# Kernel tuning notes

Measured on AMD Instinct MI355X. Metric: run time of the kernel, lower is better.

## Reference

```python
import jax, jax.numpy as jnp
import numpy as np

TAU = 0.07
EPS = 1e-12  # matches torch F.normalize clamp_min eps


def setup_inputs() -> dict:
    key = jax.random.key(0)
    k1, k2 = jax.random.split(key)
    feat = jax.random.normal(k1, (4, 64, 512, 512), dtype=jnp.float32)
    gt = jax.random.randint(k2, (4, 19, 512, 512), 0, 2, dtype=jnp.int32)
    return {"feat": feat, "gt": gt}


def reference(feat, gt):
    # feat: [b, c, h, w], gt: [b, k, h, w] multi-hot in {0,1}
    mask = (gt == 1).astype(feat.dtype)                      # [b,k,h,w]
    num_pos = mask.sum()

    # Scatter-sum class prototypes: k0[k] = sum of feat at positive pixels of class k
    k0 = jnp.einsum('bkhw,bchw->kc', mask, feat)             # [k,c]
    k0n = k0 / jnp.maximum(jnp.linalg.norm(k0, axis=1, keepdims=True), EPS)

    # Per-pixel L2-normalized features over channel dim
    fn = feat / jnp.maximum(jnp.linalg.norm(feat, axis=1, keepdims=True), EPS)

    # Cosine similarity to every prototype, temperature-scaled softmax NLL over classes
    logits = jnp.einsum('kc,bchw->bkhw', k0n, fn) / TAU      # [b,k,h,w]
    logp = jax.nn.log_softmax(logits, axis=1)

    # Sum NLL over all (pixel, class) positive pairs; a pixel positive for
    # multiple classes contributes once per class, exactly like the loop.
    loss = -(mask * logp).sum() / num_pos
    return loss
```

## Files before the change

### kernel.cpp

```cpp
#include <hip/hip_runtime.h>
#include <cstdint>
#include <cstddef>

#define HW    262144
#define C     64
#define K     19
#define NPIX  1048576
#define TAUINV (1.0f / 0.07f)
#define EPS   1e-12f

#define NCHUNK (NPIX / 32)
#define CPB    8192
#define G1     1024


typedef __attribute__((ext_vector_type(8))) short bf16x8;
typedef __attribute__((ext_vector_type(4))) float f32x4;

__device__ __forceinline__ float wave_reduce_f32(float v) {
#pragma unroll
    for (int off = 32; off; off >>= 1) v += __shfl_down(v, off);
    return v;
}
__device__ __forceinline__ unsigned wave_reduce_u32(unsigned v) {
#pragma unroll
    for (int off = 32; off; off >>= 1) v += __shfl_down(v, off);
    return v;
}

__device__ __forceinline__ void split1(float f, short& h, short& l) {
    const unsigned u  = __float_as_uint(f);
    const unsigned hb = (u + 0x7FFFu + ((u >> 16) & 1u)) & 0xFFFF0000u;
    h = (short)(hb >> 16);
    const float lo = f - __uint_as_float(hb);
    const unsigned v = __float_as_uint(lo);
    l = (short)((v + 0x7FFFu + ((v >> 16) & 1u)) >> 16);
}

__global__ __launch_bounds__(256) void k1_proto(
    const float* __restrict__ feat, const int* __restrict__ gt,
    unsigned* __restrict__ pm,
    float* __restrict__ k0p, unsigned* __restrict__ num_pos)
{
    __shared__ float red[32 * 64];
    const int tid  = threadIdx.x;
    const int lane = tid & 63;
    const int wv   = tid >> 6;
    const int q    = lane >> 4;
    const int n    = lane & 15;
    const int q8   = q << 3;

    f32x4 acc[2][4];
#pragma unroll
    for (int mt = 0; mt < 2; ++mt)
#pragma unroll
        for (int nt = 0; nt < 4; ++nt)
            acc[mt][nt] = (f32x4){0.f, 0.f, 0.f, 0.f};
    unsigned npos = 0;

    const int wave_id = blockIdx.x * 4 + wv;
    const int nwaves  = G1 * 4;

    for (int chunk = wave_id; chunk < NCHUNK; chunk += nwaves) {
        const int b   = chunk >> 13;
        const int hw0 = (chunk & (CPB - 1)) << 5;
        const size_t fbase = (size_t)b * C * HW + hw0;

        unsigned mymask = 0;
        if (lane < 32) {
            const int* gp = gt + (size_t)b * K * HW + hw0 + lane;
#pragma unroll
            for (int k = 0; k < K; ++k)
                mymask |= (gp[(size_t)k * HW] == 1) ? (1u << k) : 0u;
            pm[(size_t)chunk * 32 + lane] = mymask;
            npos += __popc(mymask);
        }

        unsigned w8[8];
#pragma unroll
        for (int j = 0; j < 8; ++j) w8[j] = __shfl(mymask, q8 + j);
        bf16x8 a0, a1;
#pragma unroll
        for (int j = 0; j < 8; ++j) {
            a0[j] = (short)(((w8[j] >> n) & 1u) * 0x3F80u);
            a1[j] = (short)(((w8[j] >> (n + 16)) & 1u) * 0x3F80u);
        }

        const float* fp = feat + fbase + (size_t)n * HW + q8;
#pragma unroll
        for (int nt = 0; nt < 4; ++nt) {
            const float* p = fp + (size_t)(nt * 16) * HW;
            const float4 x = *(const float4*)p;
            const float4 y = *(const float4*)(p + 4);
            bf16x8 bh, bl;
            {
                short h, l;
                split1(x.x, h, l); bh[0] = h; bl[0] = l;
                split1(x.y, h, l); bh[1] = h; bl[1] = l;
                split1(x.z, h, l); bh[2] = h; bl[2] = l;
                split1(x.w, h, l); bh[3] = h; bl[3] = l;
                split1(y.x, h, l); bh[4] = h; bl[4] = l;
                split1(y.y, h, l); bh[5] = h; bl[5] = l;
                split1(y.z, h, l); bh[6] = h; bl[6] = l;
                split1(y.w, h, l); bh[7] = h; bl[7] = l;
            }
            acc[0][nt] = __builtin_amdgcn_mfma_f32_16x16x32_bf16(a0, bh, acc[0][nt], 0, 0, 0);
            acc[0][nt] = __builtin_amdgcn_mfma_f32_16x16x32_bf16(a0, bl, acc[0][nt], 0, 0, 0);
            acc[1][nt] = __builtin_amdgcn_mfma_f32_16x16x32_bf16(a1, bh, acc[1][nt], 0, 0, 0);
            acc[1][nt] = __builtin_amdgcn_mfma_f32_16x16x32_bf16(a1, bl, acc[1][nt], 0, 0, 0);
        }
    }

    for (int w = 0; w < 4; ++w) {
        if (wv == w) {
#pragma unroll
            for (int mt = 0; mt < 2; ++mt)
#pragma unroll
                for (int nt = 0; nt < 4; ++nt)
#pragma unroll
                    for (int r = 0; r < 4; ++r) {
                        const int idx = (mt * 16 + q * 4 + r) * 64 + nt * 16 + n;
                        if (w == 0) red[idx]  = acc[mt][nt][r];
                        else        red[idx] += acc[mt][nt][r];
                    }
        }
        __syncthreads();
    }
    for (int i = tid; i < 32 * 64; i += 256)
        atomicAdd(&k0p[i], red[i]);

    const unsigned np = wave_reduce_u32(npos);
    if (lane == 0) atomicAdd(num_pos, np);
}

__global__ __launch_bounds__(256) void k2_norm(
    const float* __restrict__ k0p, float* __restrict__ k0n)
{
    __shared__ float rn[K];
    const int tid  = threadIdx.x;
    const int lane = tid & 63;
    const int wv   = tid >> 6;
    for (int cls = wv; cls < K; cls += 4) {
        const float v = k0p[cls * 64 + lane];
        const float s = wave_reduce_f32(v * v);
        if (lane == 0) rn[cls] = 1.0f / fmaxf(sqrtf(s), EPS);
    }
    __syncthreads();
    for (int i = tid; i < K * 64; i += 256) k0n[i] = k0p[i] * rn[i >> 6];
}

__global__ __launch_bounds__(256) void k3_loss(
    const float* __restrict__ feat, const int* __restrict__ gt,
    const unsigned* __restrict__ pm, const float* __restrict__ k0n,
    float* __restrict__ loss_sum)
{
    __shared__ __align__(16) float w[K * 64];
    const int tid = threadIdx.x;
    for (int i = tid; i < K * 64; i += 256) w[i] = k0n[i];
    __syncthreads();

    const int px0 = (blockIdx.x * 256 + tid) << 2;
    const int b   = px0 >> 18;
    const int hw  = px0 & (HW - 1);
    const float* fb = feat + (size_t)b * C * HW + hw;

    unsigned marr[4];
    {
        const uint4 mv = *(const uint4*)(pm + px0);
        marr[0] = mv.x; marr[1] = mv.y; marr[2] = mv.z; marr[3] = mv.w;
    }

    float4 dot[K];
#pragma unroll
    for (int k = 0; k < K; ++k) dot[k] = make_float4(0.f, 0.f, 0.f, 0.f);
    float4 ss = make_float4(0.f, 0.f, 0.f, 0.f);

    float4 f[8];
#pragma unroll
    for (int j = 0; j < 8; ++j)
        f[j] = *(const float4*)(fb + (size_t)j * HW);

#pragma unroll
    for (int cg = 0; cg < 64; cg += 8) {
        float4 g[8];
        if (cg + 8 < 64) {
#pragma unroll
            for (int j = 0; j < 8; ++j)
                g[j] = *(const float4*)(fb + (size_t)(cg + 8 + j) * HW);
        }
#pragma unroll
        for (int j = 0; j < 8; ++j) {
            const float4 fv = f[j];
            ss.x = fmaf(fv.x, fv.x, ss.x); ss.y = fmaf(fv.y, fv.y, ss.y);
            ss.z = fmaf(fv.z, fv.z, ss.z); ss.w = fmaf(fv.w, fv.w, ss.w);
        }
#pragma unroll
        for (int k = 0; k < K; ++k) {
            const float4 wa = *(const float4*)&w[k * 64 + cg];
            const float4 wb = *(const float4*)&w[k * 64 + cg + 4];
            float4 d = dot[k];
            d.x = fmaf(f[0].x, wa.x, d.x); d.y = fmaf(f[0].y, wa.x, d.y);
            d.z = fmaf(f[0].z, wa.x, d.z); d.w = fmaf(f[0].w, wa.x, d.w);
            d.x = fmaf(f[1].x, wa.y, d.x); d.y = fmaf(f[1].y, wa.y, d.y);
            d.z = fmaf(f[1].z, wa.y, d.z); d.w = fmaf(f[1].w, wa.y, d.w);
            d.x = fmaf(f[2].x, wa.z, d.x); d.y = fmaf(f[2].y, wa.z, d.y);
            d.z = fmaf(f[2].z, wa.z, d.z); d.w = fmaf(f[2].w, wa.z, d.w);
            d.x = fmaf(f[3].x, wa.w, d.x); d.y = fmaf(f[3].y, wa.w, d.y);
            d.z = fmaf(f[3].z, wa.w, d.z); d.w = fmaf(f[3].w, wa.w, d.w);
            d.x = fmaf(f[4].x, wb.x, d.x); d.y = fmaf(f[4].y, wb.x, d.y);
            d.z = fmaf(f[4].z, wb.x, d.z); d.w = fmaf(f[4].w, wb.x, d.w);
            d.x = fmaf(f[5].x, wb.y, d.x); d.y = fmaf(f[5].y, wb.y, d.y);
            d.z = fmaf(f[5].z, wb.y, d.z); d.w = fmaf(f[5].w, wb.y, d.w);
            d.x = fmaf(f[6].x, wb.z, d.x); d.y = fmaf(f[6].y, wb.z, d.y);
            d.z = fmaf(f[6].z, wb.z, d.z); d.w = fmaf(f[6].w, wb.z, d.w);
            d.x = fmaf(f[7].x, wb.w, d.x); d.y = fmaf(f[7].y, wb.w, d.y);
            d.z = fmaf(f[7].z, wb.w, d.z); d.w = fmaf(f[7].w, wb.w, d.w);
            dot[k] = d;
        }
        if (cg + 8 < 64) {
#pragma unroll
            for (int j = 0; j < 8; ++j) f[j] = g[j];
        }
    }

    float ls = 0.0f;
    float* dp = (float*)&dot[0];
    const float* sp = (const float*)&ss;
#pragma unroll
    for (int comp = 0; comp < 4; ++comp) {
        const float sc = TAUINV / fmaxf(sqrtf(sp[comp]), EPS);
        float mx = -1e30f;
#pragma unroll
        for (int k = 0; k < K; ++k) {
            dp[k * 4 + comp] *= sc;
            mx = fmaxf(mx, dp[k * 4 + comp]);
        }
        float se = 0.0f;
#pragma unroll
        for (int k = 0; k < K; ++k) se += expf(dp[k * 4 + comp] - mx);
        const float logZ = mx + logf(se);
        const unsigned m = marr[comp];
        ls += (float)__popc(m) * logZ;
#pragma unroll
        for (int k = 0; k < K; ++k) {
            const int s = ((int)(m << (31 - k))) >> 31;
            ls -= __int_as_float(s & __float_as_int(dp[k * 4 + comp]));
        }
    }

    ls = wave_reduce_f32(ls);
    if ((tid & 63) == 0) atomicAdd(loss_sum, ls);
}

__global__ void k4_final(const float* __restrict__ loss_sum,
                         const unsigned* __restrict__ num_pos,
                         float* __restrict__ out)
{
    out[0] = loss_sum[0] / (float)num_pos[0];
}

extern "C" void kernel_launch(void* const* d_in, const int* in_sizes, int n_in,
                              void* d_out, int out_size, void* d_ws, size_t ws_size,
                              hipStream_t stream)
{
    const float* feat = (const float*)d_in[0];
    const int*   gt   = (const int*)d_in[1];
    float*       out  = (float*)d_out;

    char* ws = (char*)d_ws;
    unsigned* num_pos  = (unsigned*)(ws + 0);
    float*    loss_sum = (float*)(ws + 4);
    float*    k0p      = (float*)(ws + 256);
    float*    k0n      = (float*)(ws + 8448);
    unsigned* pm       = (unsigned*)(ws + 65536);

    hipMemsetAsync(d_ws, 0, 16384, stream);

    k1_proto<<<G1, 256, 0, stream>>>(feat, gt, pm, k0p, num_pos);
    k2_norm <<<1,  256, 0, stream>>>(k0p, k0n);
    k3_loss <<<NPIX / 1024, 256, 0, stream>>>(feat, gt, pm, k0n, loss_sum);
    k4_final<<<1, 1, 0, stream>>>(loss_sum, num_pos, out);
}
```

Before: 535.5 us.

## Stage 128-pixel feat/gt tiles in LDS with coalesced float4 loads in prototype kernel

The prototype-accumulation kernel now has each block load a 128-pixel tile of all 64 feature channels and 19 gt planes into shared memory using row-wise float4 loads, instead of each wave issuing strided 32-pixel gathers straight from global memory. Each block handles a contiguous run of tiles within one batch, the grid is halved and a min-blocks-per-CU hint is added to launch bounds. The final atomics are reduced to the 19 real class rows, and num_pos goes through one atomic per block. The cost is more LDS use and two barriers per tile, which may limit occupancy and loses overlap between the loads and the MFMA work.

```diff
diff --git a/kernel.cpp b/kernel.cpp
--- a/kernel.cpp
+++ b/kernel.cpp
@@ -9,9 +9,11 @@
 #define TAUINV (1.0f / 0.07f)
 #define EPS   1e-12f
 
-#define NCHUNK (NPIX / 32)
-#define CPB    8192
-#define G1     1024
+#define TPX   128
+#define NTILE (NPIX / TPX)
+#define TPB   (HW / TPX)
+#define G1    512
+#define TILES_PER_BLOCK (NTILE / G1)
 
 
 typedef __attribute__((ext_vector_type(8))) short bf16x8;
@@ -37,18 +39,24 @@
     l = (short)((v + 0x7FFFu + ((v >> 16) & 1u)) >> 16);
 }
 
-__global__ __launch_bounds__(256) void k1_proto(
+__global__ __launch_bounds__(256, 3) void k1_proto(
     const float* __restrict__ feat, const int* __restrict__ gt,
     unsigned* __restrict__ pm,
     float* __restrict__ k0p, unsigned* __restrict__ num_pos)
 {
+    __shared__ __align__(16) float ftile[64][TPX];
+    __shared__ __align__(16) int   gtile[20][TPX];
     __shared__ float red[32 * 64];
+    __shared__ unsigned nps[4];
+
     const int tid  = threadIdx.x;
     const int lane = tid & 63;
     const int wv   = tid >> 6;
     const int q    = lane >> 4;
     const int n    = lane & 15;
     const int q8   = q << 3;
+    const int half = lane >> 5;
+    const int i2   = lane & 31;
 
     f32x4 acc[2][4];
 #pragma unroll
@@ -58,21 +66,55 @@
             acc[mt][nt] = (f32x4){0.f, 0.f, 0.f, 0.f};
     unsigned npos = 0;
 
-    const int wave_id = blockIdx.x * 4 + wv;
-    const int nwaves  = G1 * 4;
-
-    for (int chunk = wave_id; chunk < NCHUNK; chunk += nwaves) {
-        const int b   = chunk >> 13;
-        const int hw0 = (chunk & (CPB - 1)) << 5;
-        const size_t fbase = (size_t)b * C * HW + hw0;
+    const int T0 = blockIdx.x * TILES_PER_BLOCK;
+    const int b  = T0 >> 11;
+    const float* fB = feat + (size_t)b * C * HW;
+    const int*   gB = gt   + (size_t)b * K * HW;
+
+    for (int t = 0; t < TILES_PER_BLOCK; ++t) {
+        const int T   = T0 + t;
+        const int px0 = (T & (TPB - 1)) << 7;
+
+        float4 fr[8];
+#pragma unroll
+        for (int ii = 0; ii < 8; ++ii) {
+            const int row = 2 * (wv + 4 * ii) + half;
+            fr[ii] = *(const float4*)(fB + (size_t)row * HW + px0 + i2 * 4);
+        }
+        int4 gr[3];
+        const int ngt = (wv < 2) ? 3 : 2;
+#pragma unroll
+        for (int jj = 0; jj < 3; ++jj) {
+            if (jj < ngt) {
+                const int j   = wv + 4 * jj;
+                const int row = 2 * j + half;
+                const int srow = row > 18 ? 18 : row;
+                gr[jj] = *(const int4*)(gB + (size_t)srow * HW + px0 + i2 * 4);
+            }
+        }
+#pragma unroll
+        for (int ii = 0; ii < 8; ++ii) {
+            const int row = 2 * (wv + 4 * ii) + half;
+            *(float4*)&ftile[row][i2 * 4] = fr[ii];
+        }
+#pragma unroll
+        for (int jj = 0; jj < 3; ++jj) {
+            if (jj < ngt) {
+                const int row = 2 * (wv + 4 * jj) + half;
+                *(int4*)&gtile[row][i2 * 4] = gr[jj];
+            }
+        }
+        __syncthreads();
 
         unsigned mymask = 0;
+        {
+            const int px = wv * 32 + (lane & 31);
+#pragma unroll
+            for (int k = 0; k < K; ++k)
+                mymask |= (gtile[k][px] == 1) ? (1u << k) : 0u;
+        }
         if (lane < 32) {
-            const int* gp = gt + (size_t)b * K * HW + hw0 + lane;
-#pragma unroll
-            for (int k = 0; k < K; ++k)
-                mymask |= (gp[(size_t)k * HW] == 1) ? (1u << k) : 0u;
-            pm[(size_t)chunk * 32 + lane] = mymask;
+            pm[(size_t)T * TPX + wv * 32 + lane] = mymask;
             npos += __popc(mymask);
         }
 
@@ -86,10 +128,9 @@
             a1[j] = (short)(((w8[j] >> (n + 16)) & 1u) * 0x3F80u);
         }
 
-        const float* fp = feat + fbase + (size_t)n * HW + q8;
 #pragma unroll
         for (int nt = 0; nt < 4; ++nt) {
-            const float* p = fp + (size_t)(nt * 16) * HW;
+            const float* p = &ftile[nt * 16 + n][wv * 32 + q8];
             const float4 x = *(const float4*)p;
             const float4 y = *(const float4*)(p + 4);
             bf16x8 bh, bl;
@@ -109,6 +150,12 @@
             acc[1][nt] = __builtin_amdgcn_mfma_f32_16x16x32_bf16(a1, bh, acc[1][nt], 0, 0, 0);
             acc[1][nt] = __builtin_amdgcn_mfma_f32_16x16x32_bf16(a1, bl, acc[1][nt], 0, 0, 0);
         }
+        __syncthreads();
+    }
+
+    {
+        const unsigned np = wave_reduce_u32(npos);
+        if (lane == 0) nps[wv] = np;
     }
 
     for (int w = 0; w < 4; ++w) {
@@ -126,11 +173,10 @@
         }
         __syncthreads();
     }
-    for (int i = tid; i < 32 * 64; i += 256)
+    for (int i = tid; i < K * 64; i += 256)
         atomicAdd(&k0p[i], red[i]);
-
-    const unsigned np = wave_reduce_u32(npos);
-    if (lane == 0) atomicAdd(num_pos, np);
+    if (tid == 0)
+        atomicAdd(num_pos, nps[0] + nps[1] + nps[2] + nps[3]);
 }
 
 __global__ __launch_bounds__(256) void k2_norm(
```

Result: no change. 533.1 us (-0.4%).
